# Kernel optimization log

Measured on AMD Instinct MI355X. Metric: run time of the kernel, lower is better.

The kernel has to match this reference:

```python
import jax, jax.numpy as jnp
import numpy as np

N = 50000      # nodes
E = 800000     # edges (before self loops)
NFEAT = 128
HEADS = 4
NCLASS = 32    # per-head out channels of each GATConv
NHID = HEADS * NCLASS  # 128, inter-layer width
NEG_SLOPE = 0.2


def setup_inputs() -> dict:
    key = jax.random.key(0)
    ks = jax.random.split(key, 10)
    x = jax.random.normal(ks[0], (N, NFEAT), dtype=jnp.float32)
    adj = jax.random.randint(ks[1], (2, E), 0, N, dtype=jnp.int32)

    def glorot(k, shape):
        fan = shape[0] + shape[-1]
        return jax.random.normal(k, shape, dtype=jnp.float32) * jnp.sqrt(2.0 / fan)

    # conv1: nfeat -> heads*nclass
    W1 = glorot(ks[2], (NFEAT, HEADS * NCLASS))
    att_src1 = glorot(ks[3], (HEADS, NCLASS))
    att_dst1 = glorot(ks[4], (HEADS, NCLASS))
    b1 = jnp.zeros((HEADS * NCLASS,), dtype=jnp.float32)
    # conv2: nhid -> heads*nclass
    W2 = glorot(ks[5], (NHID, HEADS * NCLASS))
    att_src2 = glorot(ks[6], (HEADS, NCLASS))
    att_dst2 = glorot(ks[7], (HEADS, NCLASS))
    b2 = jnp.zeros((HEADS * NCLASS,), dtype=jnp.float32)
    return {"x": x, "adj": adj,
            "W1": W1, "att_src1": att_src1, "att_dst1": att_dst1, "b1": b1,
            "W2": W2, "att_src2": att_src2, "att_dst2": att_dst2, "b2": b2}


def gat_conv(x, src, dst, n, W, att_src, att_dst, bias):
    """PyG GATConv (concat=True, inference): gather -> edge attention -> segment softmax -> scatter."""
    H, C = att_src.shape
    h = (x @ W).reshape(n, H, C)                    # [N,H,C]
    a_s = jnp.sum(h * att_src[None], axis=-1)       # [N,H]
    a_d = jnp.sum(h * att_dst[None], axis=-1)       # [N,H]
    e = jax.nn.leaky_relu(a_s[src] + a_d[dst], NEG_SLOPE)  # [E,H]
    # numerically-stable segment softmax over edges grouped by destination node
    m = jax.ops.segment_max(e, dst, num_segments=n)        # [N,H]
    m = jnp.where(jnp.isfinite(m), m, 0.0)
    ex = jnp.exp(e - m[dst])                               # [E,H]
    denom = jax.ops.segment_sum(ex, dst, num_segments=n)   # [N,H]
    alpha = ex / (denom[dst] + 1e-16)                      # [E,H]
    out = jax.ops.segment_sum(h[src] * alpha[:, :, None], dst, num_segments=n)  # [N,H,C]
    return out.reshape(n, H * C) + bias


def reference(x, adj, W1, att_src1, att_dst1, b1, W2, att_src2, att_dst2, b2):
    # PyG GATConv adds self loops by default
    loops = jnp.arange(N, dtype=adj.dtype)
    src = jnp.concatenate([adj[0], loops])
    dst = jnp.concatenate([adj[1], loops])
    h = jax.nn.relu(gat_conv(x, src, dst, N, W1, att_src1, att_dst1, b1))
    # dropout is identity in eval mode
    out = gat_conv(h, src, dst, N, W2, att_src2, att_dst2, b2)
    return out
```

## Files before the change

### kernel.cpp

```cpp
#include <hip/hip_runtime.h>
#include <hip/hip_fp16.h>

#define N_NODES 50000
#define E_EDGES 800000
#define ETOT    (E_EDGES + N_NODES)
#define NF      128
#define HEADS   4
#define NC      32
#define LOG2E   1.44269504088896340736f
#define ASTRIDE 136
#define CAP     96

#define NBUCK   196
#define EPB     4096
#define NBLKA   ((ETOT + EPB - 1) / EPB)
#define PARTN   (NBUCK * NBLKA)
#define NBLKS   ((PARTN + 255) / 256)

typedef __attribute__((ext_vector_type(8))) short short8v;
typedef __attribute__((ext_vector_type(4))) float f32x4;

__device__ inline ushort rne_bf16(float x) {
    uint u = __float_as_uint(x);
    return (ushort)((u + 0x7fff + ((u >> 16) & 1)) >> 16);
}
__device__ inline float h2f_lo(uint u) { return __half2float(__ushort_as_half((ushort)(u & 0xffffu))); }
__device__ inline float h2f_hi(uint u) { return __half2float(__ushort_as_half((ushort)(u >> 16))); }

__global__ __launch_bounds__(256) void pass_hist_kernel(const int* __restrict__ adj,
                                                        int* __restrict__ partials) {
    __shared__ int lc[NBUCK];
    int tid = threadIdx.x;
    for (int i = tid; i < NBUCK; i += 256) lc[i] = 0;
    __syncthreads();
    int base = blockIdx.x * EPB;
    #pragma unroll
    for (int i = 0; i < EPB / 256; ++i) {
        int e = base + i * 256 + tid;
        if (e < ETOT) {
            int dst = (e < E_EDGES) ? adj[E_EDGES + e] : (e - E_EDGES);
            atomicAdd(&lc[dst >> 8], 1);
        }
    }
    __syncthreads();
    for (int i = tid; i < NBUCK; i += 256) partials[i * NBLKA + blockIdx.x] = lc[i];
}

__device__ inline int block_incl_scan(int v, int* sh4) {
    int lane = threadIdx.x & 63, wid = threadIdx.x >> 6;
    int s = v;
    #pragma unroll
    for (int ofs = 1; ofs < 64; ofs <<= 1) {
        int t = __shfl_up(s, ofs);
        if (lane >= ofs) s += t;
    }
    if (lane == 63) sh4[wid] = s;
    __syncthreads();
    int add = 0;
    #pragma unroll
    for (int k = 0; k < 3; ++k) if (k < wid) add += sh4[k];
    return s + add;
}

__global__ __launch_bounds__(256) void bsum2_kernel(const int* __restrict__ partials,
                                                    int* __restrict__ bsum) {
    __shared__ int sh4[4];
    int i = blockIdx.x * 256 + threadIdx.x;
    int v = (i < PARTN) ? partials[i] : 0;
    int s = block_incl_scan(v, sh4);
    if (threadIdx.x == 255) bsum[blockIdx.x] = s;
}

__global__ __launch_bounds__(256) void scan_bsums2_kernel(const int* __restrict__ bsum,
                                                          int* __restrict__ bofs) {
    __shared__ int sh4[4];
    int i = threadIdx.x;
    int v = (i < NBLKS) ? bsum[i] : 0;
    int s = block_incl_scan(v, sh4);
    if (i < NBLKS) bofs[i] = s - v;
}

__global__ __launch_bounds__(256) void scan_final2_kernel(const int* __restrict__ partials,
                                                          const int* __restrict__ bofs,
                                                          int* __restrict__ pscan) {
    __shared__ int sh4[4];
    int i = blockIdx.x * 256 + threadIdx.x;
    int v = (i < PARTN) ? partials[i] : 0;
    int s = block_incl_scan(v, sh4);
    if (i < PARTN) pscan[i] = bofs[blockIdx.x] + s - v;
}

__global__ __launch_bounds__(256) void pass_scatter_kernel(const int* __restrict__ adj,
                                                           const int* __restrict__ pscan,
                                                           int2* __restrict__ ebuf) {
    __shared__ int lc[NBUCK];
    int tid = threadIdx.x;
    for (int i = tid; i < NBUCK; i += 256) lc[i] = 0;
    __syncthreads();
    int base = blockIdx.x * EPB;
    #pragma unroll
    for (int i = 0; i < EPB / 256; ++i) {
        int e = base + i * 256 + tid;
        if (e < ETOT) {
            int src, dst;
            if (e < E_EDGES) { src = adj[e]; dst = adj[E_EDGES + e]; }
            else             { src = dst = e - E_EDGES; }
            int b = dst >> 8;
            int r = atomicAdd(&lc[b], 1);
            ebuf[pscan[b * NBLKA + blockIdx.x] + r] = make_int2(src, dst);
        }
    }
}

__global__ __launch_bounds__(256) void pass_build_kernel(const int2* __restrict__ ebuf,
                                                         const int* __restrict__ pscan,
                                                         int* __restrict__ cnt,
                                                         int* __restrict__ slots) {
    __shared__ int lc[256];
    int tid = threadIdx.x;
    int b = blockIdx.x;
    lc[tid] = 0;
    __syncthreads();
    int base = pscan[b * NBLKA];
    int end  = (b == NBUCK - 1) ? ETOT : pscan[(b + 1) * NBLKA];
    for (int e = base + tid; e < end; e += 256) {
        int2 sd = ebuf[e];
        int d = sd.y & 255;
        int r = atomicAdd(&lc[d], 1);
        slots[(size_t)sd.y * CAP + r] = sd.x;
    }
    __syncthreads();
    int dst = b * 256 + tid;
    if (dst < N_NODES) cnt[dst] = lc[tid];
}

__global__ __launch_bounds__(256) void wconv_kernel(const float* __restrict__ W,
                                                    const float* __restrict__ att_src,
                                                    const float* __restrict__ att_dst,
                                                    ushort* __restrict__ Wt) {
    int b = blockIdx.x, tid = threadIdx.x;
    if (b < 64) {
        int i = b * 256 + tid;
        int k = i >> 7, n = i & 127;
        Wt[n * 144 + k] = rne_bf16(W[i]);
    } else {
        for (int j = tid; j < 1024; j += 256) {
            int k = j >> 3, o = j & 7;
            int h = o & 3;
            const float* av = (o < 4) ? att_src : att_dst;
            float s = 0.f;
            #pragma unroll
            for (int c = 0; c < 32; ++c) s += W[k * 128 + h * 32 + c] * av[h * 32 + c];
            Wt[(128 + o) * 144 + k] = rne_bf16(s * LOG2E);
        }
        for (int j = tid; j < 8 * 144; j += 256)
            Wt[(136 + (j / 144)) * 144 + (j % 144)] = 0;
    }
}

__global__ __launch_bounds__(256) void gemm_mfma_kernel(const float* __restrict__ X,
                                                        const ushort* __restrict__ Wt,
                                                        ushort* __restrict__ Hf,
                                                        float* __restrict__ a_s,
                                                        float* __restrict__ a_d, int nrows) {
    __shared__ ushort Abf[64 * ASTRIDE];
    int tid = threadIdx.x;
    int r0 = blockIdx.x * 64;

    {
        const float4* Xv = (const float4*)(X + (size_t)r0 * NF);
        int rleft = nrows - r0;
        #pragma unroll
        for (int p = 0; p < 8; ++p) {
            int i = p * 256 + tid;
            int row = i >> 5, c4 = i & 31;
            float4 v = (row < rleft) ? Xv[row * 32 + c4] : make_float4(0.f, 0.f, 0.f, 0.f);
            ushort4 hv;
            hv.x = rne_bf16(v.x); hv.y = rne_bf16(v.y);
            hv.z = rne_bf16(v.z); hv.w = rne_bf16(v.w);
            *(ushort4*)&Abf[row * ASTRIDE + c4 * 4] = hv;
        }
    }
    __syncthreads();

    int wv = tid >> 6;
    int l = tid & 63;
    int lr = l & 15;
    int lk = l >> 4;
    int rowb = wv * 16;

    short8v a[4];
    #pragma unroll
    for (int kc = 0; kc < 4; ++kc)
        a[kc] = *(const short8v*)&Abf[(rowb + lr) * ASTRIDE + kc * 32 + lk * 8];

    f32x4 acc[9];
    #pragma unroll
    for (int ct = 0; ct < 9; ++ct) acc[ct] = (f32x4){0.f, 0.f, 0.f, 0.f};

    #pragma unroll
    for (int ct = 0; ct < 9; ++ct) {
        #pragma unroll
        for (int kc = 0; kc < 4; ++kc) {
            short8v b = *(const short8v*)&Wt[(ct * 16 + lr) * 144 + kc * 32 + lk * 8];
            acc[ct] = __builtin_amdgcn_mfma_f32_16x16x32_bf16(a[kc], b, acc[ct], 0, 0, 0);
        }
    }

    int rbase = r0 + rowb + lk * 4;
    #pragma unroll
    for (int ct = 0; ct < 8; ++ct) {
        int col = ct * 16 + lr;
        #pragma unroll
        for (int ri = 0; ri < 4; ++ri) {
            int r = rbase + ri;
            if (r < nrows) Hf[(size_t)r * NF + col] = __half_as_ushort(__float2half(acc[ct][ri]));
        }
    }
    if (lr < 8) {
        #pragma unroll
        for (int ri = 0; ri < 4; ++ri) {
            int r = rbase + ri;
            if (r < nrows) {
                if (lr < 4) a_s[(size_t)r * 4 + lr] = acc[8][ri];
                else        a_d[(size_t)r * 4 + (lr - 4)] = acc[8][ri];
            }
        }
    }
}

__global__ __launch_bounds__(256) void agg_kernel(const ushort* __restrict__ Hf,
                                                  const float* __restrict__ a_s,
                                                  const float* __restrict__ a_d,
                                                  const int* __restrict__ cnt,
                                                  const int* __restrict__ slots,
                                                  const float* __restrict__ bias,
                                                  float* __restrict__ Out, int relu) {
    int lane = threadIdx.x & 63;
    int node = blockIdx.x * 4 + (threadIdx.x >> 6);
    if (node >= N_NODES) return;
    int q = lane >> 4;
    int t = lane & 15;
    int h = t >> 2;
    float adn = a_d[node * 4 + h];
    int deg = cnt[node];
    const int* row = slots + (size_t)node * CAP;
    const uint4* H4 = (const uint4*)Hf;
    float acc[8];
    #pragma unroll
    for (int k = 0; k < 8; ++k) acc[k] = 0.f;
    float denom = 0.f;

    for (int j = 0; j < deg; j += 16) {
        int sv[4]; float ev[4]; uint4 hv[4]; bool ok[4];
        #pragma unroll
        for (int u = 0; u < 4; ++u) {
            int idx = j + u * 4 + q;
            ok[u] = idx < deg;
            sv[u] = row[ok[u] ? idx : 0];
        }
        #pragma unroll
        for (int u = 0; u < 4; ++u) ev[u] = a_s[sv[u] * 4 + h];
        #pragma unroll
        for (int u = 0; u < 4; ++u) hv[u] = H4[(size_t)sv[u] * 16 + t];
        #pragma unroll
        for (int u = 0; u < 4; ++u) {
            float e = ev[u] + adn;
            e = (e > 0.f) ? e : 0.2f * e;
            float w = ok[u] ? exp2f(e) : 0.f;
            denom += w;
            acc[0] = fmaf(h2f_lo(hv[u].x), w, acc[0]);
            acc[1] = fmaf(h2f_hi(hv[u].x), w, acc[1]);
            acc[2] = fmaf(h2f_lo(hv[u].y), w, acc[2]);
            acc[3] = fmaf(h2f_hi(hv[u].y), w, acc[3]);
            acc[4] = fmaf(h2f_lo(hv[u].z), w, acc[4]);
            acc[5] = fmaf(h2f_hi(hv[u].z), w, acc[5]);
            acc[6] = fmaf(h2f_lo(hv[u].w), w, acc[6]);
            acc[7] = fmaf(h2f_hi(hv[u].w), w, acc[7]);
        }
    }
    #pragma unroll
    for (int ofs = 16; ofs < 64; ofs <<= 1) {
        denom += __shfl_xor(denom, ofs);
        #pragma unroll
        for (int k = 0; k < 8; ++k) acc[k] += __shfl_xor(acc[k], ofs);
    }
    if (q == 0) {
        float inv = 1.f / (denom + 1e-16f);
        float4 b0 = ((const float4*)bias)[t * 2];
        float4 b1 = ((const float4*)bias)[t * 2 + 1];
        float4 o0 = make_float4(acc[0] * inv + b0.x, acc[1] * inv + b0.y,
                                acc[2] * inv + b0.z, acc[3] * inv + b0.w);
        float4 o1 = make_float4(acc[4] * inv + b1.x, acc[5] * inv + b1.y,
                                acc[6] * inv + b1.z, acc[7] * inv + b1.w);
        if (relu) {
            o0.x = fmaxf(o0.x, 0.f); o0.y = fmaxf(o0.y, 0.f);
            o0.z = fmaxf(o0.z, 0.f); o0.w = fmaxf(o0.w, 0.f);
            o1.x = fmaxf(o1.x, 0.f); o1.y = fmaxf(o1.y, 0.f);
            o1.z = fmaxf(o1.z, 0.f); o1.w = fmaxf(o1.w, 0.f);
        }
        float4* orow = (float4*)(Out + (size_t)node * NF);
        orow[t * 2]     = o0;
        orow[t * 2 + 1] = o1;
    }
}

extern "C" void kernel_launch(void* const* d_in, const int* in_sizes, int n_in,
                              void* d_out, int out_size, void* d_ws, size_t ws_size,
                              hipStream_t stream) {
    const float* x        = (const float*)d_in[0];
    const int*   adj      = (const int*)  d_in[1];
    const float* W1       = (const float*)d_in[2];
    const float* att_src1 = (const float*)d_in[3];
    const float* att_dst1 = (const float*)d_in[4];
    const float* b1       = (const float*)d_in[5];
    const float* W2       = (const float*)d_in[6];
    const float* att_src2 = (const float*)d_in[7];
    const float* att_dst2 = (const float*)d_in[8];
    const float* b2       = (const float*)d_in[9];
    float* out = (float*)d_out;

    float* obuf = (float*)d_ws;
    float* a_s  = obuf + (size_t)N_NODES * NF;
    float* a_d  = a_s + (size_t)N_NODES * HEADS;
    ushort* Hf  = (ushort*)(a_d + (size_t)N_NODES * HEADS);
    ushort* Wt  = Hf + (size_t)N_NODES * NF;
    int* cnt     = (int*)(Wt + 144 * 144);
    int* slots   = cnt + N_NODES;
    int* partials= slots + (size_t)N_NODES * CAP;
    int* pscan   = partials + PARTN;
    int* bsum    = pscan + PARTN;
    int* bofs    = bsum + NBLKS;
    int2* ebuf   = (int2*)(bofs + NBLKS + 2);

    pass_hist_kernel<<<NBLKA, 256, 0, stream>>>(adj, partials);
    bsum2_kernel<<<NBLKS, 256, 0, stream>>>(partials, bsum);
    scan_bsums2_kernel<<<1, 256, 0, stream>>>(bsum, bofs);
    scan_final2_kernel<<<NBLKS, 256, 0, stream>>>(partials, bofs, pscan);
    pass_scatter_kernel<<<NBLKA, 256, 0, stream>>>(adj, pscan, ebuf);
    pass_build_kernel<<<NBUCK, 256, 0, stream>>>(ebuf, pscan, cnt, slots);

    wconv_kernel<<<65, 256, 0, stream>>>(W1, att_src1, att_dst1, Wt);
    gemm_mfma_kernel<<<(N_NODES + 63) / 64, 256, 0, stream>>>(x, Wt, Hf, a_s, a_d, N_NODES);
    agg_kernel<<<(N_NODES + 3) / 4, 256, 0, stream>>>(Hf, a_s, a_d, cnt, slots, b1, obuf, 1);

    wconv_kernel<<<65, 256, 0, stream>>>(W2, att_src2, att_dst2, Wt);
    gemm_mfma_kernel<<<(N_NODES + 63) / 64, 256, 0, stream>>>(obuf, Wt, Hf, a_s, a_d, N_NODES);
    agg_kernel<<<(N_NODES + 3) / 4, 256, 0, stream>>>(Hf, a_s, a_d, cnt, slots, b2, out, 0);
}
```

Baseline: 161.9 us.

## Merge weight conversion into histogram kernel and halve aggregation unroll

Both layers' weight conversions now run as extra blocks in the histogram kernel, writing into two separate weight buffers. This removes two kernel launches and the serial dependency they put before each GEMM. Separately, the aggregation edge loop now processes 8 edges per iteration with 2 gathers in flight instead of 16 with 4. That lowers register use and may raise occupancy, but it exposes less memory-level parallelism per wave and less tail waste on low-degree nodes.

```diff
diff --git a/kernel.cpp b/kernel.cpp
--- a/kernel.cpp
+++ b/kernel.cpp
@@ -16,6 +16,7 @@
 #define NBLKA   ((ETOT + EPB - 1) / EPB)
 #define PARTN   (NBUCK * NBLKA)
 #define NBLKS   ((PARTN + 255) / 256)
+#define WCB     65
 
 typedef __attribute__((ext_vector_type(8))) short short8v;
 typedef __attribute__((ext_vector_type(4))) float f32x4;
@@ -27,120 +28,12 @@
 __device__ inline float h2f_lo(uint u) { return __half2float(__ushort_as_half((ushort)(u & 0xffffu))); }
 __device__ inline float h2f_hi(uint u) { return __half2float(__ushort_as_half((ushort)(u >> 16))); }
 
-__global__ __launch_bounds__(256) void pass_hist_kernel(const int* __restrict__ adj,
-                                                        int* __restrict__ partials) {
-    __shared__ int lc[NBUCK];
-    int tid = threadIdx.x;
-    for (int i = tid; i < NBUCK; i += 256) lc[i] = 0;
-    __syncthreads();
-    int base = blockIdx.x * EPB;
-    #pragma unroll
-    for (int i = 0; i < EPB / 256; ++i) {
-        int e = base + i * 256 + tid;
-        if (e < ETOT) {
-            int dst = (e < E_EDGES) ? adj[E_EDGES + e] : (e - E_EDGES);
-            atomicAdd(&lc[dst >> 8], 1);
-        }
-    }
-    __syncthreads();
-    for (int i = tid; i < NBUCK; i += 256) partials[i * NBLKA + blockIdx.x] = lc[i];
-}
-
-__device__ inline int block_incl_scan(int v, int* sh4) {
-    int lane = threadIdx.x & 63, wid = threadIdx.x >> 6;
-    int s = v;
-    #pragma unroll
-    for (int ofs = 1; ofs < 64; ofs <<= 1) {
-        int t = __shfl_up(s, ofs);
-        if (lane >= ofs) s += t;
-    }
-    if (lane == 63) sh4[wid] = s;
-    __syncthreads();
-    int add = 0;
-    #pragma unroll
-    for (int k = 0; k < 3; ++k) if (k < wid) add += sh4[k];
-    return s + add;
-}
-
-__global__ __launch_bounds__(256) void bsum2_kernel(const int* __restrict__ partials,
-                                                    int* __restrict__ bsum) {
-    __shared__ int sh4[4];
-    int i = blockIdx.x * 256 + threadIdx.x;
-    int v = (i < PARTN) ? partials[i] : 0;
-    int s = block_incl_scan(v, sh4);
-    if (threadIdx.x == 255) bsum[blockIdx.x] = s;
-}
-
-__global__ __launch_bounds__(256) void scan_bsums2_kernel(const int* __restrict__ bsum,
-                                                          int* __restrict__ bofs) {
-    __shared__ int sh4[4];
-    int i = threadIdx.x;
-    int v = (i < NBLKS) ? bsum[i] : 0;
-    int s = block_incl_scan(v, sh4);
-    if (i < NBLKS) bofs[i] = s - v;
-}
-
-__global__ __launch_bounds__(256) void scan_final2_kernel(const int* __restrict__ partials,
-                                                          const int* __restrict__ bofs,
-                                                          int* __restrict__ pscan) {
-    __shared__ int sh4[4];
-    int i = blockIdx.x * 256 + threadIdx.x;
-    int v = (i < PARTN) ? partials[i] : 0;
-    int s = block_incl_scan(v, sh4);
-    if (i < PARTN) pscan[i] = bofs[blockIdx.x] + s - v;
-}
-
-__global__ __launch_bounds__(256) void pass_scatter_kernel(const int* __restrict__ adj,
-                                                           const int* __restrict__ pscan,
-                                                           int2* __restrict__ ebuf) {
-    __shared__ int lc[NBUCK];
-    int tid = threadIdx.x;
-    for (int i = tid; i < NBUCK; i += 256) lc[i] = 0;
-    __syncthreads();
-    int base = blockIdx.x * EPB;
-    #pragma unroll
-    for (int i = 0; i < EPB / 256; ++i) {
-        int e = base + i * 256 + tid;
-        if (e < ETOT) {
-            int src, dst;
-            if (e < E_EDGES) { src = adj[e]; dst = adj[E_EDGES + e]; }
-            else             { src = dst = e - E_EDGES; }
-            int b = dst >> 8;
-            int r = atomicAdd(&lc[b], 1);
-            ebuf[pscan[b * NBLKA + blockIdx.x] + r] = make_int2(src, dst);
-        }
-    }
-}
-
-__global__ __launch_bounds__(256) void pass_build_kernel(const int2* __restrict__ ebuf,
-                                                         const int* __restrict__ pscan,
-                                                         int* __restrict__ cnt,
-                                                         int* __restrict__ slots) {
-    __shared__ int lc[256];
-    int tid = threadIdx.x;
-    int b = blockIdx.x;
-    lc[tid] = 0;
-    __syncthreads();
-    int base = pscan[b * NBLKA];
-    int end  = (b == NBUCK - 1) ? ETOT : pscan[(b + 1) * NBLKA];
-    for (int e = base + tid; e < end; e += 256) {
-        int2 sd = ebuf[e];
-        int d = sd.y & 255;
-        int r = atomicAdd(&lc[d], 1);
-        slots[(size_t)sd.y * CAP + r] = sd.x;
-    }
-    __syncthreads();
-    int dst = b * 256 + tid;
-    if (dst < N_NODES) cnt[dst] = lc[tid];
-}
-
-__global__ __launch_bounds__(256) void wconv_kernel(const float* __restrict__ W,
-                                                    const float* __restrict__ att_src,
-                                                    const float* __restrict__ att_dst,
-                                                    ushort* __restrict__ Wt) {
-    int b = blockIdx.x, tid = threadIdx.x;
-    if (b < 64) {
-        int i = b * 256 + tid;
+__device__ inline void wconv_body(int wb, int tid, const float* __restrict__ W,
+                                  const float* __restrict__ att_src,
+                                  const float* __restrict__ att_dst,
+                                  ushort* __restrict__ Wt) {
+    if (wb < 64) {
+        int i = wb * 256 + tid;
         int k = i >> 7, n = i & 127;
         Wt[n * 144 + k] = rne_bf16(W[i]);
     } else {
@@ -156,6 +49,127 @@
         for (int j = tid; j < 8 * 144; j += 256)
             Wt[(136 + (j / 144)) * 144 + (j % 144)] = 0;
     }
+}
+
+__global__ __launch_bounds__(256) void prep_kernel(const int* __restrict__ adj,
+                                                   int* __restrict__ partials,
+                                                   const float* __restrict__ W1,
+                                                   const float* __restrict__ as1,
+                                                   const float* __restrict__ ad1,
+                                                   ushort* __restrict__ Wt1,
+                                                   const float* __restrict__ W2,
+                                                   const float* __restrict__ as2,
+                                                   const float* __restrict__ ad2,
+                                                   ushort* __restrict__ Wt2) {
+    __shared__ int lc[NBUCK];
+    int b = blockIdx.x, tid = threadIdx.x;
+    if (b < NBLKA) {
+        for (int i = tid; i < NBUCK; i += 256) lc[i] = 0;
+        __syncthreads();
+        int base = b * EPB;
+        #pragma unroll
+        for (int i = 0; i < EPB / 256; ++i) {
+            int e = base + i * 256 + tid;
+            if (e < ETOT) {
+                int dst = (e < E_EDGES) ? adj[E_EDGES + e] : (e - E_EDGES);
+                atomicAdd(&lc[dst >> 8], 1);
+            }
+        }
+        __syncthreads();
+        for (int i = tid; i < NBUCK; i += 256) partials[i * NBLKA + b] = lc[i];
+    } else {
+        int wb = b - NBLKA;
+        if (wb < WCB) wconv_body(wb, tid, W1, as1, ad1, Wt1);
+        else          wconv_body(wb - WCB, tid, W2, as2, ad2, Wt2);
+    }
+}
+
+__device__ inline int block_incl_scan(int v, int* sh4) {
+    int lane = threadIdx.x & 63, wid = threadIdx.x >> 6;
+    int s = v;
+    #pragma unroll
+    for (int ofs = 1; ofs < 64; ofs <<= 1) {
+        int t = __shfl_up(s, ofs);
+        if (lane >= ofs) s += t;
+    }
+    if (lane == 63) sh4[wid] = s;
+    __syncthreads();
+    int add = 0;
+    #pragma unroll
+    for (int k = 0; k < 3; ++k) if (k < wid) add += sh4[k];
+    return s + add;
+}
+
+__global__ __launch_bounds__(256) void bsum2_kernel(const int* __restrict__ partials,
+                                                    int* __restrict__ bsum) {
+    __shared__ int sh4[4];
+    int i = blockIdx.x * 256 + threadIdx.x;
+    int v = (i < PARTN) ? partials[i] : 0;
+    int s = block_incl_scan(v, sh4);
+    if (threadIdx.x == 255) bsum[blockIdx.x] = s;
+}
+
+__global__ __launch_bounds__(256) void scan_bsums2_kernel(const int* __restrict__ bsum,
+                                                          int* __restrict__ bofs) {
+    __shared__ int sh4[4];
+    int i = threadIdx.x;
+    int v = (i < NBLKS) ? bsum[i] : 0;
+    int s = block_incl_scan(v, sh4);
+    if (i < NBLKS) bofs[i] = s - v;
+}
+
+__global__ __launch_bounds__(256) void scan_final2_kernel(const int* __restrict__ partials,
+                                                          const int* __restrict__ bofs,
+                                                          int* __restrict__ pscan) {
+    __shared__ int sh4[4];
+    int i = blockIdx.x * 256 + threadIdx.x;
+    int v = (i < PARTN) ? partials[i] : 0;
+    int s = block_incl_scan(v, sh4);
+    if (i < PARTN) pscan[i] = bofs[blockIdx.x] + s - v;
+}
+
+__global__ __launch_bounds__(256) void pass_scatter_kernel(const int* __restrict__ adj,
+                                                           const int* __restrict__ pscan,
+                                                           int2* __restrict__ ebuf) {
+    __shared__ int lc[NBUCK];
+    int tid = threadIdx.x;
+    for (int i = tid; i < NBUCK; i += 256) lc[i] = 0;
+    __syncthreads();
+    int base = blockIdx.x * EPB;
+    #pragma unroll
+    for (int i = 0; i < EPB / 256; ++i) {
+        int e = base + i * 256 + tid;
+        if (e < ETOT) {
+            int src, dst;
+            if (e < E_EDGES) { src = adj[e]; dst = adj[E_EDGES + e]; }
+            else             { src = dst = e - E_EDGES; }
+            int b = dst >> 8;
+            int r = atomicAdd(&lc[b], 1);
+            ebuf[pscan[b * NBLKA + blockIdx.x] + r] = make_int2(src, dst);
+        }
+    }
+}
+
+__global__ __launch_bounds__(256) void pass_build_kernel(const int2* __restrict__ ebuf,
+                                                         const int* __restrict__ pscan,
+                                                         int* __restrict__ cnt,
+                                                         int* __restrict__ slots) {
+    __shared__ int lc[256];
+    int tid = threadIdx.x;
+    int b = blockIdx.x;
+    lc[tid] = 0;
+    __syncthreads();
+    int base = pscan[b * NBLKA];
+    int end  = (b == NBUCK - 1) ? ETOT : pscan[(b + 1) * NBLKA];
+    for (int e = base + tid; e < end; e += 256) {
+        int2 sd = ebuf[e];
+        int d = sd.y & 255;
+        int r = atomicAdd(&lc[d], 1);
+        slots[(size_t)sd.y * CAP + r] = sd.x;
+    }
+    __syncthreads();
+    int dst = b * 256 + tid;
+    if (dst < N_NODES) cnt[dst] = lc[tid];
 }
 
 __global__ __launch_bounds__(256) void gemm_mfma_kernel(const float* __restrict__ X,
@@ -251,20 +265,20 @@
     for (int k = 0; k < 8; ++k) acc[k] = 0.f;
     float denom = 0.f;
 
-    for (int j = 0; j < deg; j += 16) {
-        int sv[4]; float ev[4]; uint4 hv[4]; bool ok[4];
-        #pragma unroll
-        for (int u = 0; u < 4; ++u) {
+    for (int j = 0; j < deg; j += 8) {
+        int sv[2]; float ev[2]; uint4 hv[2]; bool ok[2];
+        #pragma unroll
+        for (int u = 0; u < 2; ++u) {
             int idx = j + u * 4 + q;
             ok[u] = idx < deg;
             sv[u] = row[ok[u] ? idx : 0];
         }
         #pragma unroll
-        for (int u = 0; u < 4; ++u) ev[u] = a_s[sv[u] * 4 + h];
-        #pragma unroll
-        for (int u = 0; u < 4; ++u) hv[u] = H4[(size_t)sv[u] * 16 + t];
-        #pragma unroll
-        for (int u = 0; u < 4; ++u) {
+        for (int u = 0; u < 2; ++u) ev[u] = a_s[sv[u] * 4 + h];
+        #pragma unroll
+        for (int u = 0; u < 2; ++u) hv[u] = H4[(size_t)sv[u] * 16 + t];
+        #pragma unroll
+        for (int u = 0; u < 2; ++u) {
             float e = ev[u] + adn;
             e = (e > 0.f) ? e : 0.2f * e;
             float w = ok[u] ? exp2f(e) : 0.f;
@@ -324,8 +338,9 @@
     float* a_s  = obuf + (size_t)N_NODES * NF;
     float* a_d  = a_s + (size_t)N_NODES * HEADS;
     ushort* Hf  = (ushort*)(a_d + (size_t)N_NODES * HEADS);
-    ushort* Wt  = Hf + (size_t)N_NODES * NF;
-    int* cnt     = (int*)(Wt + 144 * 144);
+    ushort* Wt1 = Hf + (size_t)N_NODES * NF;
+    ushort* Wt2 = Wt1 + 144 * 144;
+    int* cnt     = (int*)(Wt2 + 144 * 144);
     int* slots   = cnt + N_NODES;
     int* partials= slots + (size_t)N_NODES * CAP;
     int* pscan   = partials + PARTN;
@@ -333,18 +348,18 @@
     int* bofs    = bsum + NBLKS;
     int2* ebuf   = (int2*)(bofs + NBLKS + 2);
 
-    pass_hist_kernel<<<NBLKA, 256, 0, stream>>>(adj, partials);
+    prep_kernel<<<NBLKA + 2 * WCB, 256, 0, stream>>>(adj, partials,
+                                                     W1, att_src1, att_dst1, Wt1,
+                                                     W2, att_src2, att_dst2, Wt2);
     bsum2_kernel<<<NBLKS, 256, 0, stream>>>(partials, bsum);
     scan_bsums2_kernel<<<1, 256, 0, stream>>>(bsum, bofs);
     scan_final2_kernel<<<NBLKS, 256, 0, stream>>>(partials, bofs, pscan);
     pass_scatter_kernel<<<NBLKA, 256, 0, stream>>>(adj, pscan, ebuf);
     pass_build_kernel<<<NBUCK, 256, 0, stream>>>(ebuf, pscan, cnt, slots);
 
-    wconv_kernel<<<65, 256, 0, stream>>>(W1, att_src1, att_dst1, Wt);
-    gemm_mfma_kernel<<<(N_NODES + 63) / 64, 256, 0, stream>>>(x, Wt, Hf, a_s, a_d, N_NODES);
+    gemm_mfma_kernel<<<(N_NODES + 63) / 64, 256, 0, stream>>>(x, Wt1, Hf, a_s, a_d, N_NODES);
     agg_kernel<<<(N_NODES + 3) / 4, 256, 0, stream>>>(Hf, a_s, a_d, cnt, slots, b1, obuf, 1);
 
-    wconv_kernel<<<65, 256, 0, stream>>>(W2, att_src2, att_dst2, Wt);
-    gemm_mfma_kernel<<<(N_NODES + 63) / 64, 256, 0, stream>>>(obuf, Wt, Hf, a_s, a_d, N_NODES);
+    gemm_mfma_kernel<<<(N_NODES + 63) / 64, 256, 0, stream>>>(obuf, Wt2, Hf, a_s, a_d, N_NODES);
     agg_kernel<<<(N_NODES + 3) / 4, 256, 0, stream>>>(Hf, a_s, a_d, cnt, slots, b2, out, 0);
 }
```

Result: faster. 149.7 us (-7.6%).
